# Kernel tuning notes

Hardware: AMD Instinct MI355X
Metric: run time of the kernel (lower is better)

The kernel has to match this reference:

```python
import jax, jax.numpy as jnp
import numpy as np
from jax import lax

# dims: batch, depth, height, width, in-channels
B, D, H, W, C = 1, 48, 48, 48, 8
K = 3          # cubic kernel size
R = 2          # n_radial_profiles = K//2 + 1
DEG = 3        # max_degree
NH = (DEG + 1) ** 2   # n_harmonics = 16
OUT = 16       # out_channels (filters)


def setup_inputs() -> dict:
    key = jax.random.key(0)
    ks = jax.random.split(key, 6)
    return {
        "x": jax.random.normal(ks[0], (B, D, H, W, C), jnp.float32),
        "atoms_real": jax.random.normal(ks[1], (K, K, K, R, NH), jnp.float32),
        "atoms_imag": jax.random.normal(ks[2], (K, K, K, R, NH), jnp.float32),
        "w": jax.random.normal(ks[3], (C, OUT, R, DEG + 1), jnp.float32) * 0.1,
        "w_center": jax.random.normal(ks[4], (C, OUT), jnp.float32) * 0.1,
        "b_center": jnp.zeros((OUT,), jnp.float32),
    }


def _depthwise_sh_conv(x, filt):
    # x: [B,D,H,W,C]; filt: [K,K,K,R,NH].  The torch code loops conv3d per input
    # channel with the SAME [K,K,K,1,R*NH] filter bank; that is exactly a
    # depthwise conv with channel multiplier R*NH and a tiled kernel.
    k = filt.shape[0]
    r, nh = filt.shape[3], filt.shape[4]
    c = x.shape[-1]
    kern = jnp.tile(filt.reshape(k, k, k, 1, r * nh), (1, 1, 1, 1, c))  # [K,K,K,1,C*R*NH], c-major
    dn = lax.conv_dimension_numbers(x.shape, kern.shape, ("NDHWC", "DHWIO", "NDHWC"))
    y = lax.conv_general_dilated(x, kern, (1, 1, 1), "SAME",
                                 dimension_numbers=dn, feature_group_count=c)
    # -> [B,D,H,W,C,R,NH]
    return y.reshape(x.shape[:4] + (c, r, nh))


def reference(x, atoms_real, atoms_imag, w, w_center, b_center):
    deg = w.shape[-1] - 1
    # repeat_interleave of per-degree weights over the 2k+1 orders of each degree
    idx = np.repeat(np.arange(deg + 1), [2 * n + 1 for n in range(deg + 1)])  # [NH]
    w_exp = w[..., idx]  # [C, OUT, R, NH]

    feat_r = _depthwise_sh_conv(x, atoms_real)  # [B,D,H,W,C,R,NH]
    feat_i = _depthwise_sh_conv(x, atoms_imag)

    # weighted reduction over input channels (axis 4) and radial profiles (axis 6)
    real = jnp.einsum("bdhwcrn,cfrn->bdhwfn", feat_r, w_exp)
    imag = jnp.einsum("bdhwcrn,cfrn->bdhwfn", feat_i, w_exp)

    # central-pixel 1x1x1 conv added to harmonic index 0 of the real part
    central = jnp.einsum("bdhwc,cf->bdhwf", x, w_center) + b_center
    real = real.at[..., 0].add(central)

    # stack real/imag feature maps: [B,D,H,W,OUT,NH,2]
    return jnp.stack([real, imag], axis=-1)
```

## Files before the change

### kernel.cpp

```cpp
#include <hip/hip_runtime.h>


typedef _Float16 half8_t __attribute__((ext_vector_type(8)));
typedef float floatx4 __attribute__((ext_vector_type(4)));

#define TB_SLOTS (7 * 32 * 64)
#define WS_BYTES_NEEDED (TB_SLOTS * 16)

__device__ inline unsigned short f2h(float v) {
    return __builtin_bit_cast(unsigned short, (_Float16)v);
}
__device__ inline unsigned pk2(float a, float b) {
    return (unsigned)f2h(a) | ((unsigned)f2h(b) << 16);
}

__global__ __launch_bounds__(512) void bsh_precompute_gemm(
    const float* __restrict__ AR,
    const float* __restrict__ AI,
    const float* __restrict__ Wgt,
    const float* __restrict__ WC,
    const float* __restrict__ Bc,
    uint4* __restrict__ TB)
{
    int s = blockIdx.x * 512 + threadIdx.x;
    if (s >= TB_SLOTS) return;
    int l = s & 63, ot = (s >> 6) & 31, t = s >> 11;
    int col = 16 * ot + (l & 15);
    int f = col >> 5, n = (col >> 1) & 15, ri = col & 1;
    int dg = (n >= 9) ? 3 : (n >= 4) ? 2 : (n >= 1) ? 1 : 0;
    const float* atom = ri ? AI : AR;
    float vj[8];
    #pragma unroll
    for (int j = 0; j < 8; ++j) {
        int kap = 32 * t + 8 * (l >> 4) + j;
        int k = kap >> 3, c = kap & 7;
        float v = 0.f;
        if (k < 27) {
            float w0 = Wgt[((c * 16 + f) * 2 + 0) * 4 + dg];
            float w1 = Wgt[((c * 16 + f) * 2 + 1) * 4 + dg];
            v = atom[k * 32 + n] * w0 + atom[k * 32 + 16 + n] * w1;
            if (k == 13 && n == 0 && ri == 0) v += WC[c * 16 + f];
        } else {
            if (c == 7 && n == 0 && ri == 0) v = Bc[f];
        }
        vj[j] = v;
    }
    TB[s] = make_uint4(pk2(vj[0], vj[1]), pk2(vj[2], vj[3]),
                       pk2(vj[4], vj[5]), pk2(vj[6], vj[7]));
}

__global__ __launch_bounds__(512) void bsh_gemm_t3(
    const float* __restrict__ X,
    const uint4* __restrict__ TB,
    float* __restrict__ Out)
{
    __shared__ _Float16 B_lds[96 * 232];

    const int tid = threadIdx.x;
    const int bid = blockIdx.x;
    const int nb = bid & 1;
    const int rb = bid >> 1;
    const int d  = rb / 24;
    const int hp = rb - 24 * d;

    const int lane = tid & 63, cg = tid >> 6;
    const int kg = lane >> 4, lr = lane & 15;

    const uint4* ap = TB + ((size_t)(nb * 16 + cg * 2) * 64 + lane);
    uint4 af[2][7];
    #pragma unroll
    for (int t = 0; t < 7; ++t) {
        af[0][t] = ap[(size_t)(t * 32 + 0) * 64];
        af[1][t] = ap[(size_t)(t * 32 + 1) * 64];
    }

    #pragma unroll
    for (int i = 0; i < 6; ++i) {
        int cell = tid + i * 512;
        if (cell < 2688) {
            int k = cell / 96;
            int v = cell - 96 * k;
            unsigned x01 = 0, x23 = 0, x45 = 0, x67 = 0;
            if (k == 27) {
                x67 = 0x3C000000u;
            } else {
                int kz = k / 9, r9 = k - 9 * kz;
                int ky = r9 / 3, kx = r9 - 3 * ky;
                int hl = (v >= 48) ? 1 : 0;
                int dd = d - 1 + kz;
                int hh = 2 * hp + hl - 1 + ky;
                int ww = v - 48 * hl - 1 + kx;
                if ((unsigned)dd < 48u && (unsigned)hh < 48u && (unsigned)ww < 48u) {
                    const float* px = &X[(((dd * 48 + hh) * 48) + ww) * 8];
                    float4 a = *(const float4*)px;
                    float4 b = *(const float4*)(px + 4);
                    x01 = pk2(a.x, a.y); x23 = pk2(a.z, a.w);
                    x45 = pk2(b.x, b.y); x67 = pk2(b.z, b.w);
                }
            }
            char* wp = (char*)B_lds + v * 464 + k * 16;
            *(uint2*)wp       = make_uint2(x01, x23);
            *(uint2*)(wp + 8) = make_uint2(x45, x67);
        }
    }
    __syncthreads();

    const char* bbase = (const char*)B_lds + lr * 464 + kg * 16;

    #pragma unroll 1
    for (int vt = 0; vt < 6; ++vt) {
        const char* brow = bbase + (size_t)vt * 16 * 464;
        half8_t b[7];
        #pragma unroll
        for (int t = 0; t < 7; ++t)
            b[t] = *(const half8_t*)(brow + 64 * t);

        floatx4 a0 = (floatx4){0.f, 0.f, 0.f, 0.f};
        floatx4 a1 = (floatx4){0.f, 0.f, 0.f, 0.f};
        #pragma unroll
        for (int t = 0; t < 7; ++t)
            a0 = __builtin_amdgcn_mfma_f32_16x16x32_f16(
                     __builtin_bit_cast(half8_t, af[0][t]), b[t], a0, 0, 0, 0);
        #pragma unroll
        for (int t = 0; t < 7; ++t)
            a1 = __builtin_amdgcn_mfma_f32_16x16x32_f16(
                     __builtin_bit_cast(half8_t, af[1][t]), b[t], a1, 0, 0, 0);

        float* ob = Out + (size_t)(rb * 96 + vt * 16 + lr) * 512
                        + nb * 256 + cg * 32 + 4 * kg;
        *(floatx4*)ob        = a0;
        *(floatx4*)(ob + 16) = a1;
    }
}

#define FB_NBLK (48*48*6)
#define FB_WS_FLOATS 5968

__global__ __launch_bounds__(512) void fb_precompute(
    const float* __restrict__ AR, const float* __restrict__ AI,
    const float* __restrict__ Wgt, const float* __restrict__ WC,
    const float* __restrict__ Bc, float* __restrict__ T)
{
    const int tid = threadIdx.x;
    for (int i = tid; i < 4096; i += 512) {
        int row = i >> 4, f = row >> 4, n = row & 15;
        int pc = (i >> 2) & 3, e = i & 3;
        int chunk = pc ^ (n & 3);
        int cr = chunk * 4 + e, c = cr >> 1, r = cr & 1;
        int dg = (n >= 9) ? 3 : (n >= 4) ? 2 : (n >= 1) ? 1 : 0;
        T[i] = Wgt[c * 128 + f * 8 + r * 4 + dg];
    }
    for (int i = tid; i < 1728; i += 512) {
        int k = i >> 6, n = (i >> 2) & 15, q = i & 3;
        const float* src = (q >> 1) ? AI : AR;
        T[4096 + i] = src[k * 32 + (q & 1) * 16 + n];
    }
    if (tid < 128) T[5824 + tid] = WC[(tid & 7) * 16 + (tid >> 3)];
    if (tid < 16)  T[5952 + tid] = Bc[tid];
}

__device__ inline float4 fb_shfl_xor4(float4 v, int m) {
    return make_float4(__shfl_xor(v.x, m), __shfl_xor(v.y, m),
                       __shfl_xor(v.z, m), __shfl_xor(v.w, m));
}

__global__ __launch_bounds__(512) void fb_kernel(
    const float* __restrict__ X, const float* __restrict__ T,
    float* __restrict__ Out)
{
    __shared__ float cst[FB_WS_FLOATS];
    __shared__ float x_lds[720];

    const int tid = threadIdx.x;
    const int bid = blockIdx.x;
    const int d  = bid / (48 * 6);
    const int r0 = bid - d * (48 * 6);
    const int h  = r0 / 6;
    const int w0 = (r0 - h * 6) * 8;

    {
        const float4* t4 = (const float4*)T;
        float4* c4 = (float4*)cst;
        #pragma unroll
        for (int i = 0; i < 3; ++i) {
            int idx = tid + i * 512;
            if (idx < FB_WS_FLOATS / 4) c4[idx] = t4[idx];
        }
        if (tid < 180) {
            int r3 = tid / 20, rem = tid - r3 * 20;
            int wx = rem >> 1, c0 = (rem & 1) * 4;
            int dz = r3 / 3, dy = r3 - dz * 3;
            int dd = d - 1 + dz, hh = h - 1 + dy, ww = w0 - 1 + wx;
            float4 v = make_float4(0.f, 0.f, 0.f, 0.f);
            if ((unsigned)dd < 48u && (unsigned)hh < 48u && (unsigned)ww < 48u)
                v = *(const float4*)&X[(((dd * 48 + hh) * 48 + ww) * 8) + c0];
            *(float4*)&x_lds[tid * 4] = v;
        }
    }
    __syncthreads();

    const int wave = tid >> 6, lane = tid & 63;
    const int n = lane & 15, g = lane >> 4;
    const float* atoms_lds = cst + 4096;
    const float* wc_lds    = cst + 5824;
    const float* b_lds     = cst + 5952;

    float sr0 = 0, sr1 = 0, sr2 = 0, sr3 = 0;
    float si0 = 0, si1 = 0, si2 = 0, si3 = 0;
    #pragma unroll
    for (int kz = 0; kz < 3; ++kz)
    #pragma unroll
    for (int ky = 0; ky < 3; ++ky)
    #pragma unroll
    for (int kx = 0; kx < 3; ++kx) {
        const int k = (kz * 3 + ky) * 3 + kx;
        const float2 xv = *(const float2*)&x_lds[(((kz * 3 + ky) * 10) + wave + kx) * 8 + 2 * g];
        const float4 a  = *(const float4*)&atoms_lds[k * 64 + n * 4];
        sr0 += xv.x * a.x; sr1 += xv.x * a.y;
        sr2 += xv.y * a.x; sr3 += xv.y * a.y;
        si0 += xv.x * a.z; si1 += xv.x * a.w;
        si2 += xv.y * a.z; si3 += xv.y * a.w;
    }
    const float4 sR0 = make_float4(sr0, sr1, sr2, sr3);
    const float4 sI0 = make_float4(si0, si1, si2, si3);
    const float4 sR1 = fb_shfl_xor4(sR0, 16), sI1 = fb_shfl_xor4(sI0, 16);
    const float4 sR2 = fb_shfl_xor4(sR0, 32), sI2 = fb_shfl_xor4(sI0, 32);
    const float4 sR3 = fb_shfl_xor4(sR1, 32), sI3 = fb_shfl_xor4(sI1, 32);

    float cent[4];
    {
        const int cb = ((1 * 3 + 1) * 10 + wave + 1) * 8;
        const float4 xc0 = *(const float4*)&x_lds[cb];
        const float4 xc1 = *(const float4*)&x_lds[cb + 4];
        #pragma unroll
        for (int fi = 0; fi < 4; ++fi) {
            const int f = 4 * g + fi;
            const float* wcr = &wc_lds[f * 8];
            cent[fi] = b_lds[f]
                + xc0.x * wcr[0] + xc0.y * wcr[1] + xc0.z * wcr[2] + xc0.w * wcr[3]
                + xc1.x * wcr[4] + xc1.y * wcr[5] + xc1.z * wcr[6] + xc1.w * wcr[7];
        }
    }

    const float4* w4 = (const float4*)cst;
    const int gx = g ^ (n & 3);
    const int out_base = ((d * 48 + h) * 48 + (w0 + wave)) * 512;
    #pragma unroll
    for (int fi = 0; fi < 4; ++fi) {
        const int f = 4 * g + fi;
        const int rb2 = (f * 16 + n) * 4;
        const float4 w0v = w4[rb2 + (gx ^ 0)];
        const float4 w1v = w4[rb2 + (gx ^ 1)];
        const float4 w2v = w4[rb2 + (gx ^ 2)];
        const float4 w3v = w4[rb2 + (gx ^ 3)];
        float accR = w0v.x*sR0.x + w0v.y*sR0.y + w0v.z*sR0.z + w0v.w*sR0.w
                   + w1v.x*sR1.x + w1v.y*sR1.y + w1v.z*sR1.z + w1v.w*sR1.w
                   + w2v.x*sR2.x + w2v.y*sR2.y + w2v.z*sR2.z + w2v.w*sR2.w
                   + w3v.x*sR3.x + w3v.y*sR3.y + w3v.z*sR3.z + w3v.w*sR3.w;
        float accI = w0v.x*sI0.x + w0v.y*sI0.y + w0v.z*sI0.z + w0v.w*sI0.w
                   + w1v.x*sI1.x + w1v.y*sI1.y + w1v.z*sI1.z + w1v.w*sI1.w
                   + w2v.x*sI2.x + w2v.y*sI2.y + w2v.z*sI2.z + w2v.w*sI2.w
                   + w3v.x*sI3.x + w3v.y*sI3.y + w3v.z*sI3.z + w3v.w*sI3.w;
        if (n == 0) accR += cent[fi];
        *(float2*)&Out[out_base + (f * 16 + n) * 2] = make_float2(accR, accI);
    }
}

extern "C" void kernel_launch(void* const* d_in, const int* in_sizes, int n_in,
                              void* d_out, int out_size, void* d_ws, size_t ws_size,
                              hipStream_t stream) {
    (void)in_sizes; (void)n_in; (void)out_size;
    const float* x  = (const float*)d_in[0];
    const float* ar = (const float*)d_in[1];
    const float* ai = (const float*)d_in[2];
    const float* w  = (const float*)d_in[3];
    const float* wc = (const float*)d_in[4];
    const float* bc = (const float*)d_in[5];
    float* out = (float*)d_out;

    if (ws_size >= (size_t)WS_BYTES_NEEDED) {
        uint4* tb = (uint4*)d_ws;
        hipLaunchKernelGGL(bsh_precompute_gemm, dim3(28), dim3(512), 0, stream,
                           ar, ai, w, wc, bc, tb);
        hipLaunchKernelGGL(bsh_gemm_t3, dim3(2304), dim3(512), 0, stream,
                           x, tb, out);
    } else {
        float* tbl = (float*)d_ws;
        hipLaunchKernelGGL(fb_precompute, dim3(1), dim3(512), 0, stream,
                           ar, ai, w, wc, bc, tbl);
        hipLaunchKernelGGL(fb_kernel, dim3(FB_NBLK), dim3(512), 0, stream,
                           x, tbl, out);
    }
}
```

Before: 56.07 us.

## Pre-pad input to fp16 buffer and stage tiles via global_load_lds

```diff
diff --git a/kernel.cpp b/kernel.cpp
--- a/kernel.cpp
+++ b/kernel.cpp
@@ -5,7 +5,15 @@
 typedef float floatx4 __attribute__((ext_vector_type(4)));
 
 #define TB_SLOTS (7 * 32 * 64)
-#define WS_BYTES_NEEDED (TB_SLOTS * 16)
+#define TBL_BYTES (TB_SLOTS * 16)
+#define XP_OFF   TBL_BYTES
+#define XP_BYTES (50 * 50 * 50 * 16)
+#define BIAS_OFF (XP_OFF + XP_BYTES)
+#define WS_T4_BYTES (BIAS_OFF + 16)
+#define WS_T3_BYTES TBL_BYTES
+
+typedef __attribute__((address_space(1))) const unsigned int gq_t;
+typedef __attribute__((address_space(3))) unsigned int lq_t;
 
 __device__ inline unsigned short f2h(float v) {
     return __builtin_bit_cast(unsigned short, (_Float16)v);
@@ -47,6 +55,116 @@
     }
     TB[s] = make_uint4(pk2(vj[0], vj[1]), pk2(vj[2], vj[3]),
                        pk2(vj[4], vj[5]), pk2(vj[6], vj[7]));
+}
+
+__global__ __launch_bounds__(512) void bsh_xp(
+    const float* __restrict__ X, char* __restrict__ WSB)
+{
+    int idx = blockIdx.x * 512 + threadIdx.x;
+    if (idx == 0)
+        *(uint4*)(WSB + BIAS_OFF) = make_uint4(0u, 0u, 0u, 0x3C000000u);
+    if (idx >= 125000) return;
+    int dd = idx / 2500, rem = idx - dd * 2500;
+    int hh = rem / 50, ww = rem - hh * 50;
+    unsigned x01 = 0, x23 = 0, x45 = 0, x67 = 0;
+    if (dd >= 1 && dd <= 48 && hh >= 1 && hh <= 48 && ww >= 1 && ww <= 48) {
+        const float* px = &X[((((dd - 1) * 48) + (hh - 1)) * 48 + (ww - 1)) * 8];
+        float4 a = *(const float4*)px;
+        float4 b = *(const float4*)(px + 4);
+        x01 = pk2(a.x, a.y); x23 = pk2(a.z, a.w);
+        x45 = pk2(b.x, b.y); x67 = pk2(b.z, b.w);
+    }
+    *(uint4*)(WSB + XP_OFF + (size_t)idx * 16) = make_uint4(x01, x23, x45, x67);
+}
+
+__global__ __launch_bounds__(512) void bsh_gemm_t4(
+    const char* __restrict__ WSB,
+    float* __restrict__ Out)
+{
+    __shared__ __align__(16) _Float16 B_lds[2][28 * 48 * 8];
+
+    const int tid = threadIdx.x;
+    const int bid = blockIdx.x;
+    const int nb = bid & 1;
+    const int rb = bid >> 1;
+    const int d  = rb / 24;
+    const int hp = rb - 24 * d;
+
+    const uint4* TB   = (const uint4*)WSB;
+    const char*  Xp   = WSB + XP_OFF;
+    const char*  BIAS = WSB + BIAS_OFF;
+
+    const int lane = tid & 63, cg = tid >> 6;
+    const int kg = lane >> 4, lr = lane & 15;
+
+    const uint4* ap = TB + ((size_t)(nb * 16 + cg * 2) * 64 + lane);
+    uint4 af[2][7];
+    #pragma unroll
+    for (int t = 0; t < 7; ++t) {
+        af[0][t] = ap[(size_t)(t * 32 + 0) * 64];
+        af[1][t] = ap[(size_t)(t * 32 + 1) * 64];
+    }
+
+    auto stage = [&](int hf) {
+        #pragma unroll
+        for (int i = 0; i < 3; ++i) {
+            int cell = tid + i * 512;
+            if (cell < 1344) {
+                int k = cell / 48;
+                int v = cell - 48 * k;
+                const char* src;
+                if (k == 27) {
+                    src = BIAS;
+                } else {
+                    int kz = k / 9, r9 = k - 9 * kz;
+                    int ky = r9 / 3, kx = r9 - 3 * ky;
+                    int dd  = d + kz;
+                    int hhp = 2 * hp + hf + ky;
+                    int wwp = v + kx;
+                    src = Xp + (((size_t)(dd * 50 + hhp) * 50 + wwp) << 4);
+                }
+                __builtin_amdgcn_global_load_lds(
+                    (const gq_t*)src,
+                    (lq_t*)&B_lds[hf][cell * 8],
+                    16, 0, 0);
+            }
+        }
+    };
+
+    auto compute = [&](int hf) {
+        const char* bbase = (const char*)&B_lds[hf][0] + kg * 768 + lr * 16;
+        #pragma unroll 1
+        for (int vt = 0; vt < 3; ++vt) {
+            const char* brow = bbase + vt * 256;
+            half8_t b[7];
+            #pragma unroll
+            for (int t = 0; t < 7; ++t)
+                b[t] = *(const half8_t*)(brow + t * 3072);
+
+            floatx4 a0 = (floatx4){0.f, 0.f, 0.f, 0.f};
+            floatx4 a1 = (floatx4){0.f, 0.f, 0.f, 0.f};
+            #pragma unroll
+            for (int t = 0; t < 7; ++t)
+                a0 = __builtin_amdgcn_mfma_f32_16x16x32_f16(
+                         __builtin_bit_cast(half8_t, af[0][t]), b[t], a0, 0, 0, 0);
+            #pragma unroll
+            for (int t = 0; t < 7; ++t)
+                a1 = __builtin_amdgcn_mfma_f32_16x16x32_f16(
+                         __builtin_bit_cast(half8_t, af[1][t]), b[t], a1, 0, 0, 0);
+
+            float* ob = Out + (size_t)((d * 48 + 2 * hp + hf) * 48 + vt * 16 + lr) * 512
+                            + nb * 256 + cg * 32 + 4 * kg;
+            *(floatx4*)ob        = a0;
+            *(floatx4*)(ob + 16) = a1;
+        }
+    };
+
+    stage(0);
+    __syncthreads();
+    stage(1);
+    compute(0);
+    __syncthreads();
+    compute(1);
 }
 
 __global__ __launch_bounds__(512) void bsh_gemm_t3(
@@ -278,7 +396,14 @@
     const float* bc = (const float*)d_in[5];
     float* out = (float*)d_out;
 
-    if (ws_size >= (size_t)WS_BYTES_NEEDED) {
+    if (ws_size >= (size_t)WS_T4_BYTES) {
+        char* wsb = (char*)d_ws;
+        hipLaunchKernelGGL(bsh_precompute_gemm, dim3(28), dim3(512), 0, stream,
+                           ar, ai, w, wc, bc, (uint4*)wsb);
+        hipLaunchKernelGGL(bsh_xp, dim3(245), dim3(512), 0, stream, x, wsb);
+        hipLaunchKernelGGL(bsh_gemm_t4, dim3(2304), dim3(512), 0, stream,
+                           (const char*)wsb, out);
+    } else if (ws_size >= (size_t)WS_T3_BYTES) {
         uint4* tb = (uint4*)d_ws;
         hipLaunchKernelGGL(bsh_precompute_gemm, dim3(28), dim3(512), 0, stream,
                            ar, ai, w, wc, bc, tb);
```

After: 54.65 us. -2.5%, faster.
